# Optimization experiments

Measured on AMD Instinct MI355X. Metric: run time of the kernel, lower is better.

Reference implementation:

```python
import jax, jax.numpy as jnp
import numpy as np

N = 256
DT = 1.0 / 4096.0
BATCH = 256
LENGTH = 4096

def _legt_transition(n):
    # HiPPO-LegT continuous-time transition (Gu et al.)
    Q = np.arange(n, dtype=np.float64)
    R = (2.0 * Q + 1.0) ** 0.5
    j, i = np.meshgrid(Q, Q)
    A = R[:, None] * np.where(i < j, (-1.0) ** (i - j), 1.0) * R[None, :]
    B = R[:, None]
    return -A, B

def _bilinear(A, B, dt):
    # scipy cont2discrete(method='bilinear'), alpha=0.5
    n = A.shape[0]
    ima = np.eye(n) - 0.5 * dt * A
    Ad = np.linalg.solve(ima, np.eye(n) + 0.5 * dt * A)
    Bd = np.linalg.solve(ima, dt * B)
    return Ad, Bd

def setup_inputs() -> dict:
    key = jax.random.key(0)
    Ac, Bc = _legt_transition(N)
    evals = (2.0 * np.arange(N, dtype=np.float64) + 1.0) ** 0.5
    C = evals @ Ac                        # (N,) readout from continuous A
    D = np.sum(evals * Bc.squeeze(-1))    # scalar
    scale = 1.0 / (1.0 - 0.5 * D * DT)
    C_discr = (scale * 0.5 * DT * C).astype(np.float32)          # (N,)
    D_discr = np.array([scale * (1.0 + 0.5 * DT * D)], np.float32)  # (1,)
    Ad, Bd = _bilinear(Ac, Bc, DT)
    inputs = jax.random.normal(key, (BATCH, LENGTH), dtype=jnp.float32)
    return {
        "inputs": inputs,
        "A": jnp.asarray(Ad, dtype=jnp.float32),
        "B": jnp.asarray(Bd.squeeze(-1), dtype=jnp.float32),
        "C_discr": jnp.asarray(C_discr),
        "D_discr": jnp.asarray(D_discr),
    }

def reference(inputs, A, B, C_discr, D_discr):
    # inputs: (batch, length). teacher_ratio=1.0 -> fully teacher-forced LTI scan:
    #   c_t = A c_{t-1} + B * u_t ;  pred_t = fac_t * (c_t @ C) + D * u_t
    # where fac_0 = 1 and fac_t = 2 for t > 0 (as in the torch loop).
    batch, length = inputs.shape
    c0 = jnp.zeros((batch, A.shape[0]), dtype=inputs.dtype)
    facs = jnp.where(jnp.arange(length) == 0, 1.0, 2.0).astype(inputs.dtype)

    def step(c, xs):
        x_t, fac = xs                                   # x_t: (batch,)
        c = c @ A.T + B[None, :] * x_t[:, None]         # (batch, N); F.linear(c, A)
        pred = fac * (c @ C_discr) + D_discr[0] * x_t   # (batch,)
        return c, pred

    _, preds = jax.lax.scan(step, c0, (inputs.T, facs))  # preds: (length, batch)
    return preds.T  # (batch, length)
```

## Files before the change

### kernel.cpp

```cpp
#include <hip/hip_runtime.h>


#define LENGTH 4096

#define WS_P2    0
#define WS_P4    65536
#define WS_P8    131072
#define WS_P16   196608
#define WS_P32   262144
#define WS_P64T  327680
#define WS_P128T 393216
#define WS_W     458752
#define WS_V     475136
#define WS_XH    491520
#define WS_XL    1015808
#define WS_AH    1540096
#define WS_AL    1605632

typedef __attribute__((ext_vector_type(8))) short bf16x8;
typedef __attribute__((ext_vector_type(4))) float f32x4;
#define MFMA(a, b, c) __builtin_amdgcn_mfma_f32_16x16x32_bf16(a, b, c, 0, 0, 0)

__device__ inline unsigned short f2bf(float f) {
    unsigned int u = __float_as_uint(f);
    return (unsigned short)((u + 0x7FFFu + ((u >> 16) & 1u)) >> 16);
}
__device__ inline void split2(float f, short& h, short& l) {
    unsigned short hu = f2bf(f);
    float fh = __uint_as_float((unsigned int)hu << 16);
    h = (short)hu;
    l = (short)f2bf(f - fh);
}

__device__ __forceinline__ void mm_body(const float* __restrict__ X,
                                        const float* __restrict__ Y,
                                        float* __restrict__ Z,
                                        int row, int t, bool trans, float* red) {
    const int j = t & 255, p = t >> 8;
    const float* xr = X + row * 256 + 64 * p;
    const float* yc = Y + (64 * p) * 256 + j;
    float a0 = 0.f, a1 = 0.f, a2 = 0.f, a3 = 0.f;
#pragma unroll
    for (int l = 0; l < 64; l += 4) {
        a0 = fmaf(xr[l + 0], yc[(l + 0) * 256], a0);
        a1 = fmaf(xr[l + 1], yc[(l + 1) * 256], a1);
        a2 = fmaf(xr[l + 2], yc[(l + 2) * 256], a2);
        a3 = fmaf(xr[l + 3], yc[(l + 3) * 256], a3);
    }
    float s = (a0 + a1) + (a2 + a3);
    if (p) red[(p - 1) * 256 + j] = s;
    __syncthreads();
    if (!p) {
        float z = s + red[j] + red[256 + j] + red[512 + j];
        if (trans) Z[j * 256 + row] = z;
        else       Z[row * 256 + j] = z;
    }
}

__global__ __launch_bounds__(1024) void fused0(const float* __restrict__ A,
                                               const float* __restrict__ x,
                                               float* __restrict__ P2,
                                               short* __restrict__ XH,
                                               short* __restrict__ XL) {
    __shared__ float red[3 * 256];
    const int t = threadIdx.x;
    if (blockIdx.x >= 128) {
        mm_body(A, A, P2, blockIdx.x - 128, t, false, red);
        return;
    }
    const int wv = t >> 6, lane = t & 63;
    const int pj = blockIdx.x * 16 + wv;
    const int c = pj >> 4, blk = pj & 15;
    const int b = blk * 16 + (lane & 15);
    const int s0 = c * 32 + 8 * (lane >> 4);
    const float4 v0 = reinterpret_cast<const float4*>(&x[b * LENGTH + s0])[0];
    const float4 v1 = reinterpret_cast<const float4*>(&x[b * LENGTH + s0])[1];
    const float f[8] = {v0.x, v0.y, v0.z, v0.w, v1.x, v1.y, v1.z, v1.w};
    bf16x8 hv, lv;
#pragma unroll
    for (int e = 0; e < 8; ++e) {
        short h, l;
        split2(f[e], h, l);
        hv[e] = h; lv[e] = l;
    }
    const int off = (pj * 64 + lane) * 8;
    *reinterpret_cast<bf16x8*>(XH + off) = hv;
    *reinterpret_cast<bf16x8*>(XL + off) = lv;
}

__global__ __launch_bounds__(1024) void mmsq(const float* __restrict__ S,
                                             float* __restrict__ D) {
    __shared__ float red[3 * 256];
    mm_body(S, S, D, blockIdx.x, threadIdx.x, false, red);
}

__device__ __forceinline__ void rv_mm(const float* __restrict__ v,
                                      const float* __restrict__ M,
                                      float* curl, float (*red4)[256],
                                      int j, int p) {
    float s0 = 0.f, s1 = 0.f;
#pragma unroll
    for (int ii = 0; ii < 64; ii += 2) {
        s0 = fmaf(v[64 * p + ii],     M[(64 * p + ii) * 256 + j],     s0);
        s1 = fmaf(v[64 * p + ii + 1], M[(64 * p + ii + 1) * 256 + j], s1);
    }
    red4[p][j] = s0 + s1;
    __syncthreads();
    if (!p) curl[j] = red4[0][j] + red4[1][j] + red4[2][j] + red4[3][j];
    __syncthreads();
}

__global__ __launch_bounds__(1024) void p64w(const float* __restrict__ P32,
                                             float* __restrict__ P64T,
                                             const float* __restrict__ A,
                                             const float* __restrict__ C,
                                             const float* __restrict__ P16,
                                             float* __restrict__ W) {
    __shared__ float red[3 * 256];
    __shared__ float cur[256];
    __shared__ float red4[4][256];
    const int t = threadIdx.x;
    if (blockIdx.x >= 4) {
        mm_body(P32, P32, P64T, blockIdx.x - 4, t, true, red);
        return;
    }
    const int c = blockIdx.x;
    const int j = t & 255, p = t >> 8;
    float areg[64];
#pragma unroll
    for (int ii = 0; ii < 64; ++ii) areg[ii] = A[(64 * p + ii) * 256 + j];

    if (c == 0) {
        if (t < 256) cur[t] = C[t];
        __syncthreads();
    } else {
        rv_mm(C, (c == 2) ? P32 : P16, cur, red4, j, p);
        if (c == 3) rv_mm(cur, P32, cur, red4, j, p);
    }
    for (int s_ = 0; s_ < 16; ++s_) {
        if (!p) W[(16 * c + s_) * 256 + j] = cur[j];
        if (s_ == 15) break;
        float s0 = 0.f, s1 = 0.f;
#pragma unroll
        for (int m = 0; m < 16; ++m) {
            float4 c4 = *reinterpret_cast<const float4*>(&cur[64 * p + 4 * m]);
            s0 = fmaf(c4.x, areg[4 * m + 0], s0);
            s1 = fmaf(c4.y, areg[4 * m + 1], s1);
            s0 = fmaf(c4.z, areg[4 * m + 2], s0);
            s1 = fmaf(c4.w, areg[4 * m + 3], s1);
        }
        red4[p][j] = s0 + s1;
        __syncthreads();
        if (!p) cur[j] = red4[0][j] + red4[1][j] + red4[2][j] + red4[3][j];
        __syncthreads();
    }
}

__global__ __launch_bounds__(1024) void vgen(const float* __restrict__ P64T,
                                             const float* __restrict__ P128T,
                                             const float* __restrict__ B,
                                             float* __restrict__ V) {
    __shared__ float cur[256];
    __shared__ float red4[4][256];
    const int t = threadIdx.x;
    const int i = t & 255, p = t >> 8;
    const int c = blockIdx.x;
    float mreg[64];
#pragma unroll
    for (int jj = 0; jj < 64; ++jj) mreg[jj] = P128T[(64 * p + jj) * 256 + i];

    if (c == 0) {
        if (t < 256) cur[t] = B[t];
        __syncthreads();
    } else {
        float s0 = 0.f, s1 = 0.f;
#pragma unroll
        for (int jj = 0; jj < 64; jj += 2) {
            s0 = fmaf(P64T[(64 * p + jj) * 256 + i],     B[64 * p + jj],     s0);
            s1 = fmaf(P64T[(64 * p + jj + 1) * 256 + i], B[64 * p + jj + 1], s1);
        }
        red4[p][i] = s0 + s1;
        __syncthreads();
        if (!p) cur[i] = red4[0][i] + red4[1][i] + red4[2][i] + red4[3][i];
        __syncthreads();
    }
    for (int s_ = 0; s_ < 32; ++s_) {
        if (!p) V[(2 * s_ + c) * 256 + i] = cur[i];
        if (s_ == 31) break;
        float s0 = 0.f, s1 = 0.f;
#pragma unroll
        for (int m = 0; m < 16; ++m) {
            float4 c4 = *reinterpret_cast<const float4*>(&cur[64 * p + 4 * m]);
            s0 = fmaf(c4.x, mreg[4 * m + 0], s0);
            s1 = fmaf(c4.y, mreg[4 * m + 1], s1);
            s0 = fmaf(c4.z, mreg[4 * m + 2], s0);
            s1 = fmaf(c4.w, mreg[4 * m + 3], s1);
        }
        red4[p][i] = s0 + s1;
        __syncthreads();
        if (!p) cur[i] = red4[0][i] + red4[1][i] + red4[2][i] + red4[3][i];
        __syncthreads();
    }
}

__global__ __launch_bounds__(512) void kfrag(const float* __restrict__ Wm,
                                             const float* __restrict__ Vm,
                                             short* __restrict__ AH,
                                             short* __restrict__ AL) {
    const int bid = blockIdx.x, t = threadIdx.x;
    __shared__ float Wl[64 * 257];
    __shared__ float Vl[768];
    __shared__ float kl[160];
    for (int u = t; u < 16384; u += 512)
        Wl[(u >> 8) * 257 + (u & 255)] = Wm[u];
    for (int u = t; u < 768; u += 512) {
        const int q = 2 * bid - 1 + (u >> 8);
        Vl[u] = (q >= 0) ? Vm[q * 256 + (u & 255)] : 0.f;
    }
    __syncthreads();
    if (t < 159) {
        const int tau = 128 * bid - 31 + t;
        float s = 0.f;
        if (tau >= 0) {
            const int r = tau & 63;
            const int qq = (tau >> 6) - (2 * bid - 1);
            const float* wr = &Wl[r * 257];
            const float* vr = &Vl[qq * 256];
            float s0 = 0.f, s1 = 0.f, s2 = 0.f, s3 = 0.f;
#pragma unroll 8
            for (int i2 = 0; i2 < 256; i2 += 4) {
                s0 = fmaf(wr[i2 + 0], vr[i2 + 0], s0);
                s1 = fmaf(wr[i2 + 1], vr[i2 + 1], s1);
                s2 = fmaf(wr[i2 + 2], vr[i2 + 2], s2);
                s3 = fmaf(wr[i2 + 3], vr[i2 + 3], s3);
            }
            s = (s0 + s1) + (s2 + s3);
        }
        kl[t] = s;
    }
    __syncthreads();
    const int wv = t >> 6, lane = t & 63;
    const int m = 8 * bid + wv;
    bf16x8 hv, lv;
#pragma unroll
    for (int el = 0; el < 8; ++el) {
        const int rel = 16 * wv + (lane & 15) - 8 * (lane >> 4) - el + 31;
        short h_, l_;
        split2(kl[rel], h_, l_);
        hv[el] = h_; lv[el] = l_;
    }
    const int off = (m * 64 + lane) * 8;
    *reinterpret_cast<bf16x8*>(AH + off) = hv;
    *reinterpret_cast<bf16x8*>(AL + off) = lv;
}

struct Frag {
    bf16x8 bh0, bh1, bl0, bl1;
    bf16x8 ah0, ah1, ah2, ah3, al0, al1, al2, al3;
    int d0, tile;
};

#define LOADF(F, IDX_) do {                                                    \
        const int i_ = (IDX_);                                                 \
        const int tl_ = (i_ < nA) ? 0 : 1;                                     \
        const int cc_ = i_ - (tl_ ? nA : 0);                                   \
        const int xo_ = ((cc_ * 16 + bt2) * 64 + lane) * 8;                    \
        F.bh0 = *reinterpret_cast<const bf16x8*>(XH + xo_);                    \
        F.bh1 = *reinterpret_cast<const bf16x8*>(XH + xo_ + 512);              \
        F.bl0 = *reinterpret_cast<const bf16x8*>(XL + xo_);                    \
        F.bl1 = *reinterpret_cast<const bf16x8*>(XL + xo_ + 512);              \
        const int d_ = (tl_ ? tB64 : tA64) - cc_ * 32;                         \
        F.d0 = d_; F.tile = tl_;                                               \
        const int m0_ = (d_ > 0 ? d_ : 0) >> 4;                                \
        const int m1_ = (d_ + 16 > 0 ? d_ + 16 : 0) >> 4;                      \
        const int m2_ = (d_ + 32 > 0 ? d_ + 32 : 0) >> 4;                      \
        const int m3_ = (d_ + 48 > 0 ? d_ + 48 : 0) >> 4;                      \
        F.ah0 = *reinterpret_cast<const bf16x8*>(AH + (m0_ * 64 + lane) * 8);  \
        F.al0 = *reinterpret_cast<const bf16x8*>(AL + (m0_ * 64 + lane) * 8);  \
        F.ah1 = *reinterpret_cast<const bf16x8*>(AH + (m1_ * 64 + lane) * 8);  \
        F.al1 = *reinterpret_cast<const bf16x8*>(AL + (m1_ * 64 + lane) * 8);  \
        F.ah2 = *reinterpret_cast<const bf16x8*>(AH + (m2_ * 64 + lane) * 8);  \
        F.al2 = *reinterpret_cast<const bf16x8*>(AL + (m2_ * 64 + lane) * 8);  \
        F.ah3 = *reinterpret_cast<const bf16x8*>(AH + (m3_ * 64 + lane) * 8);  \
        F.al3 = *reinterpret_cast<const bf16x8*>(AL + (m3_ * 64 + lane) * 8);  \
    } while (0)

#define ONER(F, T, R, AHF, ALF)                                                \
        if (F.d0 + 16 * R >= 0) {                                              \
            acc[T][R][0] = MFMA(F.AHF, F.bh0, acc[T][R][0]);                   \
            acc[T][R][1] = MFMA(F.AHF, F.bh1, acc[T][R][1]);                   \
            acc[T][R][0] = MFMA(F.AHF, F.bl0, acc[T][R][0]);                   \
            acc[T][R][1] = MFMA(F.AHF, F.bl1, acc[T][R][1]);                   \
            acc[T][R][0] = MFMA(F.ALF, F.bh0, acc[T][R][0]);                   \
            acc[T][R][1] = MFMA(F.ALF, F.bh1, acc[T][R][1]);                   \
        }

#define APPLY(F) do {                                                          \
        if (F.tile == 0) {                                                     \
            ONER(F, 0, 0, ah0, al0) ONER(F, 0, 1, ah1, al1)                    \
            ONER(F, 0, 2, ah2, al2) ONER(F, 0, 3, ah3, al3)                    \
        } else {                                                               \
            ONER(F, 1, 0, ah0, al0) ONER(F, 1, 1, ah1, al1)                    \
            ONER(F, 1, 2, ah2, al2) ONER(F, 1, 3, ah3, al3)                    \
        }                                                                      \
    } while (0)

__global__ __launch_bounds__(512) void convm(const short* __restrict__ XH,
                                             const short* __restrict__ XL,
                                             const short* __restrict__ AH,
                                             const short* __restrict__ AL,
                                             const float* __restrict__ x,
                                             const float* __restrict__ Dp,
                                             float* __restrict__ out) {
    const int pr = blockIdx.x & 31;
    const int bt = blockIdx.x >> 5;
    const int tid = threadIdx.x;
    const int w = tid >> 6, lane = tid & 63;
    const int tA64 = pr * 64, tB64 = (63 - pr) * 64;
    const int nA = 2 * pr + 2;
    const int bt2 = bt * 2;

    __shared__ float lds[16 * 64 * 34];

    f32x4 acc[2][4][2];
#pragma unroll
    for (int t_ = 0; t_ < 2; ++t_)
#pragma unroll
        for (int r_ = 0; r_ < 4; ++r_)
#pragma unroll
            for (int c_ = 0; c_ < 2; ++c_) acc[t_][r_][c_] = f32x4{0.f, 0.f, 0.f, 0.f};

    Frag f0, f1;
    LOADF(f0, w);
    int idx = w;
    while (true) {
        const int n1 = idx + 8;
        const bool h1 = n1 < 130;
        if (h1) LOADF(f1, n1);
        APPLY(f0);
        if (!h1) break;
        const int n2 = n1 + 8;
        const bool h2 = n2 < 130;
        if (h2) LOADF(f0, n2);
        APPLY(f1);
        if (!h2) break;
        idx = n2;
    }

    const int lq = lane >> 4, lr = lane & 15;
#pragma unroll
    for (int t_ = 0; t_ < 2; ++t_)
#pragma unroll
        for (int r_ = 0; r_ < 4; ++r_)
#pragma unroll
            for (int c_ = 0; c_ < 2; ++c_)
#pragma unroll
                for (int e_ = 0; e_ < 4; ++e_)
                    lds[((w * 2 + t_) * 64 + (r_ * 16 + lq * 4 + e_)) * 34 +
                        (c_ * 16 + lr)] = acc[t_][r_][c_][e_];
    __syncthreads();

    const float D = Dp[0];
    const int b = tid >> 4;
    const int t4 = (tid & 15) * 4;
#pragma unroll
    for (int t_ = 0; t_ < 2; ++t_) {
        const int tbase = t_ ? tB64 : tA64;
        float s0 = 0.f, s1 = 0.f, s2 = 0.f, s3 = 0.f;
#pragma unroll
        for (int w_ = 0; w_ < 8; ++w_) {
            const float* lp = &lds[((w_ * 2 + t_) * 64 + t4) * 34 + b];
            s0 += lp[0]; s1 += lp[34]; s2 += lp[68]; s3 += lp[102];
        }
        const int g = (bt * 32 + b) * LENGTH + tbase + t4;
        const float4 xv = *reinterpret_cast<const float4*>(x + g);
        float4 o;
        o.x = 2.f * s0 + D * xv.x;
        o.y = 2.f * s1 + D * xv.y;
        o.z = 2.f * s2 + D * xv.z;
        o.w = 2.f * s3 + D * xv.w;
        if (tbase == 0 && t4 == 0) o.x -= s0;
        *reinterpret_cast<float4*>(out + g) = o;
    }
}

extern "C" void kernel_launch(void* const* d_in, const int* in_sizes, int n_in,
                              void* d_out, int out_size, void* d_ws, size_t ws_size,
                              hipStream_t stream) {
    const float* x  = (const float*)d_in[0];
    const float* A  = (const float*)d_in[1];
    const float* B  = (const float*)d_in[2];
    const float* C  = (const float*)d_in[3];
    const float* Dp = (const float*)d_in[4];
    float* out = (float*)d_out;
    float* ws  = (float*)d_ws;

    float* P2    = ws + WS_P2;
    float* P4    = ws + WS_P4;
    float* P8    = ws + WS_P8;
    float* P16   = ws + WS_P16;
    float* P32   = ws + WS_P32;
    float* P64T  = ws + WS_P64T;
    float* P128T = ws + WS_P128T;
    float* Wm    = ws + WS_W;
    float* Vm    = ws + WS_V;
    short* XHs   = (short*)(ws + WS_XH);
    short* XLs   = (short*)(ws + WS_XL);
    short* AHs   = (short*)(ws + WS_AH);
    short* ALs   = (short*)(ws + WS_AL);

    fused0<<<384, 1024, 0, stream>>>(A, x, P2, XHs, XLs);
    mmsq<<<256, 1024, 0, stream>>>(P2, P4);
    mmsq<<<256, 1024, 0, stream>>>(P4, P8);
    mmsq<<<256, 1024, 0, stream>>>(P8, P16);
    mmsq<<<256, 1024, 0, stream>>>(P16, P32);
    p64w<<<260, 1024, 0, stream>>>(P32, P64T, A, C, P16, Wm);
    mmsq<<<256, 1024, 0, stream>>>(P64T, P128T);
    vgen<<<2, 1024, 0, stream>>>(P64T, P128T, B, Vm);
    kfrag<<<32, 512, 0, stream>>>(Wm, Vm, AHs, ALs);
    convm<<<256, 512, 0, stream>>>(XHs, XLs, AHs, ALs, x, Dp, out);
}
```

Before: 120.5 us.

## Merge W and V vector chains into one single-wave-per-column kernel

Replaces the p64w and vgen kernels with a plain transposed squaring kernel and a new 6-block 'chains' kernel. Each thread now owns a full output column, holding 176 rows of the matrix in registers and 80 rows in LDS. This removes the 4-way cross-wave partial-sum reduction and one barrier per step. The W chains (16 steps) and V chains (32 steps) now run together after P128T, so the W chains no longer overlap with the P64T squaring. The cost is heavy register pressure (176 floats per thread) and serial 256-length dot products with only 256 threads per block.

```diff
diff --git a/kernel.cpp b/kernel.cpp
--- a/kernel.cpp
+++ b/kernel.cpp
@@ -93,112 +93,98 @@
     __shared__ float red[3 * 256];
     mm_body(S, S, D, blockIdx.x, threadIdx.x, false, red);
 }
-
-__device__ __forceinline__ void rv_mm(const float* __restrict__ v,
-                                      const float* __restrict__ M,
-                                      float* curl, float (*red4)[256],
-                                      int j, int p) {
-    float s0 = 0.f, s1 = 0.f;
-#pragma unroll
-    for (int ii = 0; ii < 64; ii += 2) {
-        s0 = fmaf(v[64 * p + ii],     M[(64 * p + ii) * 256 + j],     s0);
-        s1 = fmaf(v[64 * p + ii + 1], M[(64 * p + ii + 1) * 256 + j], s1);
-    }
-    red4[p][j] = s0 + s1;
+__global__ __launch_bounds__(1024) void mmsqT(const float* __restrict__ S,
+                                              float* __restrict__ D) {
+    __shared__ float red[3 * 256];
+    mm_body(S, S, D, blockIdx.x, threadIdx.x, true, red);
+}
+
+__global__ __launch_bounds__(256) void chains(const float* __restrict__ A,
+                                              const float* __restrict__ P16,
+                                              const float* __restrict__ P32,
+                                              const float* __restrict__ P64T,
+                                              const float* __restrict__ P128T,
+                                              const float* __restrict__ B,
+                                              const float* __restrict__ C,
+                                              float* __restrict__ Wm,
+                                              float* __restrict__ Vm) {
+    const int bidx = blockIdx.x;
+    const int j = threadIdx.x;
+    __shared__ float cur[256];
+    __shared__ __align__(16) float Alds[80][256];
+    const float* M = (bidx < 4) ? A : P128T;
+
+    float areg[176];
+#pragma unroll 4
+    for (int i = 0; i < 176; ++i) areg[i] = M[i * 256 + j];
+    for (int r = 0; r < 80; ++r) Alds[r][j] = M[(176 + r) * 256 + j];
+
+    float sv;
+    if (bidx == 0) {
+        sv = C[j];
+    } else if (bidx == 4) {
+        sv = B[j];
+    } else if (bidx == 5) {
+        float a0 = 0.f, a1 = 0.f, a2 = 0.f, a3 = 0.f;
+        for (int k = 0; k < 256; k += 4) {
+            a0 = fmaf(B[k + 0], P64T[(k + 0) * 256 + j], a0);
+            a1 = fmaf(B[k + 1], P64T[(k + 1) * 256 + j], a1);
+            a2 = fmaf(B[k + 2], P64T[(k + 2) * 256 + j], a2);
+            a3 = fmaf(B[k + 3], P64T[(k + 3) * 256 + j], a3);
+        }
+        sv = (a0 + a1) + (a2 + a3);
+    } else {
+        const float* M1 = (bidx == 2) ? P32 : P16;
+        float a0 = 0.f, a1 = 0.f, a2 = 0.f, a3 = 0.f;
+        for (int i = 0; i < 256; i += 4) {
+            a0 = fmaf(C[i + 0], M1[(i + 0) * 256 + j], a0);
+            a1 = fmaf(C[i + 1], M1[(i + 1) * 256 + j], a1);
+            a2 = fmaf(C[i + 2], M1[(i + 2) * 256 + j], a2);
+            a3 = fmaf(C[i + 3], M1[(i + 3) * 256 + j], a3);
+        }
+        sv = (a0 + a1) + (a2 + a3);
+    }
+    if (bidx == 3) {
+        cur[j] = sv;
+        __syncthreads();
+        float a0 = 0.f, a1 = 0.f, a2 = 0.f, a3 = 0.f;
+        for (int i = 0; i < 256; i += 4) {
+            a0 = fmaf(cur[i + 0], P32[(i + 0) * 256 + j], a0);
+            a1 = fmaf(cur[i + 1], P32[(i + 1) * 256 + j], a1);
+            a2 = fmaf(cur[i + 2], P32[(i + 2) * 256 + j], a2);
+            a3 = fmaf(cur[i + 3], P32[(i + 3) * 256 + j], a3);
+        }
+        sv = (a0 + a1) + (a2 + a3);
+        __syncthreads();
+    }
+    cur[j] = sv;
     __syncthreads();
-    if (!p) curl[j] = red4[0][j] + red4[1][j] + red4[2][j] + red4[3][j];
-    __syncthreads();
-}
-
-__global__ __launch_bounds__(1024) void p64w(const float* __restrict__ P32,
-                                             float* __restrict__ P64T,
-                                             const float* __restrict__ A,
-                                             const float* __restrict__ C,
-                                             const float* __restrict__ P16,
-                                             float* __restrict__ W) {
-    __shared__ float red[3 * 256];
-    __shared__ float cur[256];
-    __shared__ float red4[4][256];
-    const int t = threadIdx.x;
-    if (blockIdx.x >= 4) {
-        mm_body(P32, P32, P64T, blockIdx.x - 4, t, true, red);
-        return;
-    }
-    const int c = blockIdx.x;
-    const int j = t & 255, p = t >> 8;
-    float areg[64];
-#pragma unroll
-    for (int ii = 0; ii < 64; ++ii) areg[ii] = A[(64 * p + ii) * 256 + j];
-
-    if (c == 0) {
-        if (t < 256) cur[t] = C[t];
+
+    const int nst = (bidx < 4) ? 16 : 32;
+    for (int s = 0; s < nst; ++s) {
+        if (bidx < 4) Wm[(16 * bidx + s) * 256 + j] = cur[j];
+        else          Vm[(2 * s + (bidx - 4)) * 256 + j] = cur[j];
+        if (s == nst - 1) break;
+        float a0 = 0.f, a1 = 0.f, a2 = 0.f, a3 = 0.f;
+#pragma unroll
+        for (int i = 0; i < 176; i += 4) {
+            const float4 c4 = *reinterpret_cast<const float4*>(&cur[i]);
+            a0 = fmaf(c4.x, areg[i + 0], a0);
+            a1 = fmaf(c4.y, areg[i + 1], a1);
+            a2 = fmaf(c4.z, areg[i + 2], a2);
+            a3 = fmaf(c4.w, areg[i + 3], a3);
+        }
+#pragma unroll
+        for (int r = 0; r < 80; r += 4) {
+            const float4 c4 = *reinterpret_cast<const float4*>(&cur[176 + r]);
+            a0 = fmaf(c4.x, Alds[r + 0][j], a0);
+            a1 = fmaf(c4.y, Alds[r + 1][j], a1);
+            a2 = fmaf(c4.z, Alds[r + 2][j], a2);
+            a3 = fmaf(c4.w, Alds[r + 3][j], a3);
+        }
+        const float nv = (a0 + a1) + (a2 + a3);
         __syncthreads();
-    } else {
-        rv_mm(C, (c == 2) ? P32 : P16, cur, red4, j, p);
-        if (c == 3) rv_mm(cur, P32, cur, red4, j, p);
-    }
-    for (int s_ = 0; s_ < 16; ++s_) {
-        if (!p) W[(16 * c + s_) * 256 + j] = cur[j];
-        if (s_ == 15) break;
-        float s0 = 0.f, s1 = 0.f;
-#pragma unroll
-        for (int m = 0; m < 16; ++m) {
-            float4 c4 = *reinterpret_cast<const float4*>(&cur[64 * p + 4 * m]);
-            s0 = fmaf(c4.x, areg[4 * m + 0], s0);
-            s1 = fmaf(c4.y, areg[4 * m + 1], s1);
-            s0 = fmaf(c4.z, areg[4 * m + 2], s0);
-            s1 = fmaf(c4.w, areg[4 * m + 3], s1);
-        }
-        red4[p][j] = s0 + s1;
-        __syncthreads();
-        if (!p) cur[j] = red4[0][j] + red4[1][j] + red4[2][j] + red4[3][j];
-        __syncthreads();
-    }
-}
-
-__global__ __launch_bounds__(1024) void vgen(const float* __restrict__ P64T,
-                                             const float* __restrict__ P128T,
-                                             const float* __restrict__ B,
-                                             float* __restrict__ V) {
-    __shared__ float cur[256];
-    __shared__ float red4[4][256];
-    const int t = threadIdx.x;
-    const int i = t & 255, p = t >> 8;
-    const int c = blockIdx.x;
-    float mreg[64];
-#pragma unroll
-    for (int jj = 0; jj < 64; ++jj) mreg[jj] = P128T[(64 * p + jj) * 256 + i];
-
-    if (c == 0) {
-        if (t < 256) cur[t] = B[t];
-        __syncthreads();
-    } else {
-        float s0 = 0.f, s1 = 0.f;
-#pragma unroll
-        for (int jj = 0; jj < 64; jj += 2) {
-            s0 = fmaf(P64T[(64 * p + jj) * 256 + i],     B[64 * p + jj],     s0);
-            s1 = fmaf(P64T[(64 * p + jj + 1) * 256 + i], B[64 * p + jj + 1], s1);
-        }
-        red4[p][i] = s0 + s1;
-        __syncthreads();
-        if (!p) cur[i] = red4[0][i] + red4[1][i] + red4[2][i] + red4[3][i];
-        __syncthreads();
-    }
-    for (int s_ = 0; s_ < 32; ++s_) {
-        if (!p) V[(2 * s_ + c) * 256 + i] = cur[i];
-        if (s_ == 31) break;
-        float s0 = 0.f, s1 = 0.f;
-#pragma unroll
-        for (int m = 0; m < 16; ++m) {
-            float4 c4 = *reinterpret_cast<const float4*>(&cur[64 * p + 4 * m]);
-            s0 = fmaf(c4.x, mreg[4 * m + 0], s0);
-            s1 = fmaf(c4.y, mreg[4 * m + 1], s1);
-            s0 = fmaf(c4.z, mreg[4 * m + 2], s0);
-            s1 = fmaf(c4.w, mreg[4 * m + 3], s1);
-        }
-        red4[p][i] = s0 + s1;
-        __syncthreads();
-        if (!p) cur[i] = red4[0][i] + red4[1][i] + red4[2][i] + red4[3][i];
+        cur[j] = nv;
         __syncthreads();
     }
 }
@@ -414,9 +400,9 @@
     mmsq<<<256, 1024, 0, stream>>>(P4, P8);
     mmsq<<<256, 1024, 0, stream>>>(P8, P16);
     mmsq<<<256, 1024, 0, stream>>>(P16, P32);
-    p64w<<<260, 1024, 0, stream>>>(P32, P64T, A, C, P16, Wm);
+    mmsqT<<<256, 1024, 0, stream>>>(P32, P64T);
     mmsq<<<256, 1024, 0, stream>>>(P64T, P128T);
-    vgen<<<2, 1024, 0, stream>>>(P64T, P128T, B, Vm);
+    chains<<<6, 256, 0, stream>>>(A, P16, P32, P64T, P128T, B, C, Wm, Vm);
     kfrag<<<32, 512, 0, stream>>>(Wm, Vm, AHs, ALs);
     convm<<<256, 512, 0, stream>>>(XHs, XLs, AHs, ALs, x, Dp, out);
 }
```

Result: slower. 327.7 us (+172.0%).
